# Kernel tuning notes

Hardware: AMD Instinct MI355X
Metric: run time of the kernel (lower is better)

Reference implementation:

```python
import jax, jax.numpy as jnp
import numpy as np

HEADS = 12
D_MODEL = 768
D_K = D_MODEL // HEADS


def setup_inputs() -> dict:
    key = jax.random.key(0)
    ks = jax.random.split(key, 11)
    B, S, D = 2, 2048, D_MODEL
    s = 1.0 / np.sqrt(D)
    return {
        "query": jax.random.normal(ks[0], (B, S, D), jnp.float32),
        "key": jax.random.normal(ks[1], (B, S, D), jnp.float32),
        "value": jax.random.normal(ks[2], (B, S, D), jnp.float32),
        "Wq": jax.random.normal(ks[3], (D, D), jnp.float32) * s,
        "bq": jnp.zeros((D,), jnp.float32),
        "Wk": jax.random.normal(ks[4], (D, D), jnp.float32) * s,
        "bk": jnp.zeros((D,), jnp.float32),
        "Wv": jax.random.normal(ks[5], (D, D), jnp.float32) * s,
        "bv": jnp.zeros((D,), jnp.float32),
        "Wo": jax.random.normal(ks[6], (D, D), jnp.float32) * s,
        "bo": jnp.zeros((D,), jnp.float32),
    }


def reference(query, key, value, Wq, bq, Wk, bk, Wv, bv, Wo, bo):
    B, S, D = query.shape
    # linear projections (weights stored as [in, out])
    q = query @ Wq + bq
    k = key @ Wk + bk
    v = value @ Wv + bv
    # [B, H, S, d_k]
    q = q.reshape(B, S, HEADS, D_K).transpose(0, 2, 1, 3)
    k = k.reshape(B, S, HEADS, D_K).transpose(0, 2, 1, 3)
    v = v.reshape(B, S, HEADS, D_K).transpose(0, 2, 1, 3)
    # scores: note module scales by sqrt(d_k) (key.size(-1)), not self.scaled
    scores = jnp.einsum("bhqd,bhkd->bhqk", q, k) / jnp.sqrt(jnp.asarray(D_K, q.dtype))
    weights = jax.nn.softmax(scores, axis=-1)
    context = jnp.einsum("bhqk,bhkd->bhqd", weights, v)
    context = context.transpose(0, 2, 1, 3).reshape(B, S, D)
    return context @ Wo + bo
```

## Files before the change

### kernel.cpp

```cpp
#include <hip/hip_runtime.h>
#include <hip/hip_bf16.h>
#include <math.h>

#define D_MODEL 768
#define HEADS 12
#define DK 64
#define SEQ 2048
#define BATCH 2
#define MTOT (BATCH * SEQ)
#define QSCALE 0.18033688011112042f

using short8 = __attribute__((ext_vector_type(8))) short;
using us4    = __attribute__((ext_vector_type(4))) unsigned short;
using f32x4  = __attribute__((ext_vector_type(4))) float;
using f32x16 = __attribute__((ext_vector_type(16))) float;

static __device__ __forceinline__ unsigned f2bf2(float x, float y) {
    __hip_bfloat162 t = __float22bfloat162_rn(float2{x, y});
    return *reinterpret_cast<unsigned*>(&t);
}
static __device__ __forceinline__ unsigned short f2bf1(float x) {
    __hip_bfloat16 t = __float2bfloat16(x);
    return *reinterpret_cast<unsigned short*>(&t);
}
static __device__ __forceinline__ float bf2f(unsigned short u) {
    unsigned v = (unsigned)u << 16;
    return __uint_as_float(v);
}
static __device__ __forceinline__ short8 cvt8(float4 a, float4 b) {
    union { unsigned u[4]; short8 s; } r;
    r.u[0] = f2bf2(a.x, a.y);
    r.u[1] = f2bf2(a.z, a.w);
    r.u[2] = f2bf2(b.x, b.y);
    r.u[3] = f2bf2(b.z, b.w);
    return r.s;
}
static __device__ __forceinline__ float fast_exp2(float x) {
#if __has_builtin(__builtin_amdgcn_exp2f)
    return __builtin_amdgcn_exp2f(x);
#else
    return __expf(x * 0.6931471805599453f);
#endif
}
static __device__ __forceinline__ unsigned pk2(float lo, float hi) {
    unsigned d;
    asm("v_cvt_pk_bf16_f32 %0, %1, %2" : "=v"(d) : "v"(lo), "v"(hi));
    return d;
}

static __device__ __forceinline__ void gload_lds16(const void* g, void* l) {
    __builtin_amdgcn_global_load_lds(
        (const __attribute__((address_space(1))) void*)g,
        (__attribute__((address_space(3))) void*)l, 16, 0, 0);
}

static __device__ __forceinline__ void barrier_lgkm() {
    asm volatile("s_waitcnt lgkmcnt(0)" ::: "memory");
    __builtin_amdgcn_s_barrier();
    __builtin_amdgcn_sched_barrier(0);
}
static __device__ __forceinline__ void barrier_vm0() {
    asm volatile("s_waitcnt vmcnt(0)" ::: "memory");
    __builtin_amdgcn_s_barrier();
    __builtin_amdgcn_sched_barrier(0);
}

__global__ __launch_bounds__(256) void cvt_wt_k(
    const float* __restrict__ Wq, const float* __restrict__ Wk,
    const float* __restrict__ Wv, const float* __restrict__ Wo,
    unsigned short* __restrict__ Wqt, unsigned short* __restrict__ Wkt,
    unsigned short* __restrict__ Wvt, unsigned short* __restrict__ Wot)
{
    const int z = blockIdx.z;
    const float* W = z == 0 ? Wq : z == 1 ? Wk : z == 2 ? Wv : Wo;
    unsigned short* Wt = z == 0 ? Wqt : z == 1 ? Wkt : z == 2 ? Wvt : Wot;
    __shared__ float t[32][33];
    const int n0 = blockIdx.x * 32, k0 = blockIdx.y * 32;
    const int tx = threadIdx.x & 31;
    const int ty0 = (threadIdx.x >> 5) * 4;
    #pragma unroll
    for (int j = 0; j < 4; ++j)
        t[ty0 + j][tx] = W[(size_t)(k0 + ty0 + j) * D_MODEL + n0 + tx];
    __syncthreads();
    #pragma unroll
    for (int j = 0; j < 4; ++j)
        Wt[(size_t)(n0 + ty0 + j) * D_MODEL + k0 + tx] = f2bf1(t[tx][ty0 + j]);
}

__global__ __launch_bounds__(512) void gemm_qkv_k(
    const float* __restrict__ query, const float* __restrict__ key,
    const float* __restrict__ value,
    const unsigned short* __restrict__ Wqt, const unsigned short* __restrict__ Wkt,
    const unsigned short* __restrict__ Wvt,
    const float* __restrict__ bq, const float* __restrict__ bk,
    const float* __restrict__ bv,
    unsigned short* __restrict__ qb, unsigned short* __restrict__ kb,
    unsigned short* __restrict__ vb)
{
    __shared__ __align__(16) char gsm[65536];

    const int bid = blockIdx.x;
    const int xcd = bid & 7;
    const int idx = bid >> 3;
    const int z   = idx / 24;
    const int rr  = idx % 24;
    const int brow = (xcd * 4 + rr / 6) * 128;
    const int bcol = (rr % 6) * 128;

    const float* A           = z == 0 ? query : z == 1 ? key : value;
    const unsigned short* Wt = z == 0 ? Wqt : z == 1 ? Wkt : Wvt;
    const float* bias        = z == 0 ? bq  : z == 1 ? bk  : bv;
    unsigned short* C        = z == 0 ? qb  : z == 1 ? kb  : vb;
    const float scale        = z == 0 ? QSCALE : 1.0f;

    const int tid  = threadIdx.x;
    const int w    = tid >> 6;
    const int lane = tid & 63;
    const int g    = lane >> 4, c = lane & 15;
    const int wr   = w >> 2, wc = w & 3;

    f32x4 acc[4][2] = {};

    const int xc  = (c & 7) << 4;
    const int rb0 = c * 128 + ((g * 16) ^ xc);
    const int rb1 = c * 128 + ((64 + g * 16) ^ xc);

    int bsrow[2], bsoff[2], bsdst[2];
    #pragma unroll
    for (int r = 0; r < 2; ++r) {
        int phys = (w * 2 + r) * 1024 + lane * 16;
        int row  = phys >> 7;
        int slot = (phys >> 4) & 7;
        bsrow[r] = row;
        bsoff[r] = (slot ^ (row & 7)) * 8;
        bsdst[r] = (w * 2 + r) * 1024;
    }
    const int ar = tid >> 2;
    const int ac = (tid & 3) << 4;
    int awa[2];
    #pragma unroll
    for (int i = 0; i < 2; ++i)
        awa[i] = ar * 128 + (((ac << 1) + 16 * i) ^ ((ar & 7) << 4));
    const float* Ap32 = A + (size_t)(brow + ar) * D_MODEL + ac;

    float4 ra0, ra1, ra2, ra3;

    auto stageB = [&](int k0, int buf) {
        #pragma unroll
        for (int r = 0; r < 2; ++r)
            gload_lds16(Wt + (size_t)(bcol + bsrow[r]) * D_MODEL + k0 + bsoff[r],
                        gsm + 32768 + buf * 16384 + bsdst[r]);
    };
    auto loadA32 = [&](int k0) {
        ra0 = *(const float4*)(Ap32 + k0);
        ra1 = *(const float4*)(Ap32 + k0 + 4);
        ra2 = *(const float4*)(Ap32 + k0 + 8);
        ra3 = *(const float4*)(Ap32 + k0 + 12);
    };
    auto writeA32 = [&](int buf) {
        *(short8*)(gsm + buf * 16384 + awa[0]) = cvt8(ra0, ra1);
        *(short8*)(gsm + buf * 16384 + awa[1]) = cvt8(ra2, ra3);
    };

    stageB(0, 0);
    loadA32(0);
    writeA32(0);
    barrier_lgkm();

    for (int k0 = 0; k0 < D_MODEL; k0 += 128) {
        #pragma unroll
        for (int u = 0; u < 2; ++u) {
            const int kn = min(k0 + u * 64 + 64, D_MODEL - 64);
            stageB(kn, u ^ 1);
            loadA32(kn);
            __builtin_amdgcn_sched_barrier(0);

            __builtin_amdgcn_s_setprio(1);
            #pragma unroll
            for (int kstep = 0; kstep < 2; ++kstep) {
                const int rb = kstep ? rb1 : rb0;
                short8 af[4], bf[2];
                #pragma unroll
                for (int m = 0; m < 4; ++m)
                    af[m] = *(const short8*)(gsm + u * 16384 + wr * 8192 +
                                             m * 2048 + rb);
                #pragma unroll
                for (int n = 0; n < 2; ++n)
                    bf[n] = *(const short8*)(gsm + 32768 + u * 16384 +
                                             wc * 4096 + n * 2048 + rb);
                #pragma unroll
                for (int m = 0; m < 4; ++m)
                    #pragma unroll
                    for (int n = 0; n < 2; ++n)
                        acc[m][n] = __builtin_amdgcn_mfma_f32_16x16x32_bf16(
                                        af[m], bf[n], acc[m][n], 0, 0, 0);
            }
            __builtin_amdgcn_s_setprio(0);

            writeA32(u ^ 1);
            barrier_lgkm();
        }
    }

    #pragma unroll
    for (int m = 0; m < 4; ++m)
        #pragma unroll
        for (int n = 0; n < 2; ++n) {
            const int col = bcol + wc * 32 + n * 16 + c;
            const float bval = bias[col];
            #pragma unroll
            for (int j = 0; j < 4; ++j) {
                const int row = brow + wr * 64 + m * 16 + g * 4 + j;
                C[(size_t)row * D_MODEL + col] = f2bf1((acc[m][n][j] + bval) * scale);
            }
        }
}

__global__ __launch_bounds__(256) void gemm_o_k(
    const unsigned short* __restrict__ A, const unsigned short* __restrict__ Wt,
    const float* __restrict__ bias, float* __restrict__ C)
{
    __shared__ __align__(16) char gsm[32768];

    const int bid = blockIdx.x;
    const int xcd = bid & 7;
    const int idx = bid >> 3;
    const int brow = (xcd * 8 + idx / 12) * 64;
    const int bcol = (idx % 12) * 64;

    const int tid  = threadIdx.x;
    const int w    = tid >> 6;
    const int lane = tid & 63;
    const int g    = lane >> 4, c = lane & 15;
    const int wr   = w >> 1, wc = w & 1;

    f32x4 acc[2][2] = {{f32x4{0,0,0,0}, f32x4{0,0,0,0}},
                       {f32x4{0,0,0,0}, f32x4{0,0,0,0}}};

    const int xc  = (c & 7) << 4;
    const int rb0 = c * 128 + ((g * 16) ^ xc);
    const int rb1 = c * 128 + ((64 + g * 16) ^ xc);
    const int a0 = rb0 + wr * 4096, a1 = rb1 + wr * 4096;
    const int b0r = rb0 + 16384 + wc * 4096, b1r = rb1 + 16384 + wc * 4096;

    int bsrow[2], bsoff[2], bsdst[2];
    #pragma unroll
    for (int r = 0; r < 2; ++r) {
        int phys = (w + 4 * r) * 1024 + lane * 16;
        int row  = phys >> 7;
        int slot = (phys >> 4) & 7;
        bsrow[r] = row;
        bsoff[r] = (slot ^ (row & 7)) * 8;
        bsdst[r] = (w + 4 * r) * 1024;
    }

    auto stage = [&](int k0, int buf) {
        #pragma unroll
        for (int r = 0; r < 2; ++r) {
            gload_lds16(A  + (size_t)(brow + bsrow[r]) * D_MODEL + k0 + bsoff[r],
                        gsm + buf * 8192 + bsdst[r]);
            gload_lds16(Wt + (size_t)(bcol + bsrow[r]) * D_MODEL + k0 + bsoff[r],
                        gsm + 16384 + buf * 8192 + bsdst[r]);
        }
    };

    stage(0, 0);
    barrier_vm0();

    for (int k0 = 0; k0 < D_MODEL; k0 += 128) {
        #pragma unroll
        for (int u = 0; u < 2; ++u) {
            const int kn = min(k0 + u * 64 + 64, D_MODEL - 64);
            stage(kn, u ^ 1);
            __builtin_amdgcn_sched_barrier(0);

            #pragma unroll
            for (int kstep = 0; kstep < 2; ++kstep) {
                short8 af[2], bf[2];
                #pragma unroll
                for (int m = 0; m < 2; ++m)
                    af[m] = *(const short8*)(gsm + u * 8192 + m * 2048 +
                                             (kstep ? a1 : a0));
                #pragma unroll
                for (int n = 0; n < 2; ++n)
                    bf[n] = *(const short8*)(gsm + u * 8192 + n * 2048 +
                                             (kstep ? b1r : b0r));
                #pragma unroll
                for (int m = 0; m < 2; ++m)
                    #pragma unroll
                    for (int n = 0; n < 2; ++n)
                        acc[m][n] = __builtin_amdgcn_mfma_f32_16x16x32_bf16(
                                        af[m], bf[n], acc[m][n], 0, 0, 0);
            }
            barrier_vm0();
        }
    }

    #pragma unroll
    for (int m = 0; m < 2; ++m)
        #pragma unroll
        for (int n = 0; n < 2; ++n) {
            const int col = bcol + wc * 32 + n * 16 + c;
            const float bval = bias[col];
            #pragma unroll
            for (int j = 0; j < 4; ++j) {
                const int row = brow + wr * 32 + m * 16 + g * 4 + j;
                C[(size_t)row * D_MODEL + col] = acc[m][n][j] + bval;
            }
        }
}

__global__ __launch_bounds__(256) void attn_mfma_k(
    const unsigned short* __restrict__ q, const unsigned short* __restrict__ k,
    const unsigned short* __restrict__ v, unsigned short* __restrict__ opart,
    float* __restrict__ mpart, float* __restrict__ lpart)
{
    __shared__ __align__(16) char sm[32768];

    const int tid  = threadIdx.x;
    const int w    = tid >> 6;
    const int lane = tid & 63;
    const int c    = lane & 31;
    const int hi   = lane >> 5;

    const int bid  = blockIdx.x;
    const int swz  = (bid & 7) * 96 + (bid >> 3);
    const int qt   = swz & 15;
    const int rest = swz >> 4;
    const int half = rest & 1;
    const int hb   = rest >> 1;
    const int h    = hb % HEADS;
    const int b    = hb / HEADS;
    const int q0   = qt * 128;
    const int NT2  = 16;

    short8 qf[4];
    {
        const unsigned short* qp =
            q + (size_t)(b * SEQ + q0 + w * 32 + c) * D_MODEL + h * DK;
        #pragma unroll
        for (int t = 0; t < 4; ++t)
            qf[t] = *(const short8*)(qp + t * 16 + hi * 8);
    }

    float m_run = -INFINITY;
    f32x16 lacc = {};
    f32x16 o0 = {}, o1 = {};
    const short8 ONES = {0x3F80, 0x3F80, 0x3F80, 0x3F80,
                         0x3F80, 0x3F80, 0x3F80, 0x3F80};

    const int xc = (c & 7) << 4;
    int koff[4];
    #pragma unroll
    for (int t = 0; t < 4; ++t)
        koff[t] = ((32 * t + 16 * hi) ^ xc) + c * 128;

    int kdst[2];
    const unsigned short* kg[2];
    {
        const unsigned short* kbase =
            k + (size_t)(b * SEQ + half * (SEQ / 2)) * D_MODEL + h * DK;
        #pragma unroll
        for (int r = 0; r < 2; ++r) {
            int phys = (w + 4 * r) * 1024 + lane * 16;
            int row  = phys >> 7;
            int slot = (phys >> 4) & 7;
            kdst[r]  = (w + 4 * r) * 1024;
            kg[r]    = kbase + (size_t)row * D_MODEL + (slot ^ (row & 7)) * 8;
        }
    }
    const int cv = tid & 15, vd0 = (tid >> 4) << 2;
    const int vposP = 16 * (cv >> 3) + 8 * ((cv >> 2) & 1) + 2 * (cv & 3);
    int vwa[4];
    #pragma unroll
    for (int j = 0; j < 4; ++j) {
        const int row = vd0 + j;
        vwa[j] = 16384 + row * 128 + ((2 * vposP) ^ ((row & 7) << 4));
    }
    const unsigned short* vg =
        v + (size_t)(b * SEQ + half * (SEQ / 2) + cv) * D_MODEL + h * DK + vd0;
    const int TS = 64 * D_MODEL;

    us4 va, vb_, vc, vd;

    auto issue_k = [&](int buf) {
        gload_lds16(kg[0], sm + buf * 8192 + kdst[0]);
        gload_lds16(kg[1], sm + buf * 8192 + kdst[1]);
        kg[0] += TS; kg[1] += TS;
    };
    auto load_v = [&]() {
        va  = *(const us4*)(vg);
        vb_ = *(const us4*)(vg + 16 * D_MODEL);
        vc  = *(const us4*)(vg + 32 * D_MODEL);
        vd  = *(const us4*)(vg + 48 * D_MODEL);
        vg += TS;
    };
    auto write_v = [&](int buf) {
        #pragma unroll
        for (int j = 0; j < 4; ++j) {
            unsigned lo  = (unsigned)va[j]  | ((unsigned)vc[j] << 16);
            unsigned hi2 = (unsigned)vb_[j] | ((unsigned)vd[j] << 16);
            *(unsigned*)(sm + buf * 8192 + vwa[j])        = lo;
            *(unsigned*)(sm + buf * 8192 + (vwa[j] ^ 64)) = hi2;
        }
    };

    issue_k(0);
    __builtin_amdgcn_sched_barrier(0);
    load_v();
    write_v(0);
    barrier_lgkm();

    for (int kt2 = 0; kt2 < NT2; kt2 += 2) {
        #pragma unroll
        for (int u = 0; u < 2; ++u) {
            const int tile = kt2 + u;
            issue_k(u ^ 1);
            __builtin_amdgcn_sched_barrier(0);
            load_v();
            __builtin_amdgcn_sched_barrier(0);

            f32x16 s0 = {}, s1 = {};
            __builtin_amdgcn_s_setprio(1);
            #pragma unroll
            for (int t = 0; t < 4; ++t) {
                short8 kf0 = *(const short8*)(sm + u * 8192 + koff[t]);
                short8 kf1 = *(const short8*)(sm + u * 8192 + 4096 + koff[t]);
                s0 = __builtin_amdgcn_mfma_f32_32x32x16_bf16(kf0, qf[t], s0, 0, 0, 0);
                s1 = __builtin_amdgcn_mfma_f32_32x32x16_bf16(kf1, qf[t], s1, 0, 0, 0);
            }
            __builtin_amdgcn_s_setprio(0);

            float rmax = s0[0];
            #pragma unroll
            for (int r = 1; r < 16; ++r) rmax = fmaxf(rmax, s0[r]);
            #pragma unroll
            for (int r = 0; r < 16; ++r) rmax = fmaxf(rmax, s1[r]);
            rmax = fmaxf(rmax, __shfl_xor(rmax, 32));

            if (tile == 0) {
                m_run = rmax;
            } else if (__any(rmax > m_run + 11.0f)) {
                const float mnew = fmaxf(m_run, rmax);
                const float sc = fast_exp2(m_run - mnew);
                m_run = mnew;
                #pragma unroll
                for (int r = 0; r < 16; ++r) {
                    const float scr = __shfl(sc, (r & 3) + 8 * (r >> 2) + 4 * hi);
                    lacc[r] *= scr;
                    o0[r] *= scr;
                    o1[r] *= scr;
                }
            }

            #pragma unroll
            for (int r = 0; r < 16; ++r) {
                s0[r] = fast_exp2(s0[r] - m_run);
                s1[r] = fast_exp2(s1[r] - m_run);
            }

            __builtin_amdgcn_s_setprio(1);
            #pragma unroll
            for (int t = 0; t < 4; ++t) {
                union { unsigned u4[4]; short8 s8; } pf;
                #pragma unroll
                for (int j = 0; j < 4; ++j)
                    pf.u4[j] = pk2(s0[4 * t + j], s1[4 * t + j]);
                short8 vf0 = *(const short8*)(sm + 16384 + u * 8192 + koff[t]);
                short8 vf1 = *(const short8*)(sm + 16384 + u * 8192 + 4096 + koff[t]);
                lacc = __builtin_amdgcn_mfma_f32_32x32x16_bf16(pf.s8, ONES, lacc, 0, 0, 0);
                o0 = __builtin_amdgcn_mfma_f32_32x32x16_bf16(pf.s8, vf0, o0, 0, 0, 0);
                o1 = __builtin_amdgcn_mfma_f32_32x32x16_bf16(pf.s8, vf1, o1, 0, 0, 0);
            }
            __builtin_amdgcn_s_setprio(0);

            write_v(u ^ 1);
            barrier_lgkm();
        }
    }

    const size_t obase = (size_t)half * ((size_t)MTOT * D_MODEL) +
                         (size_t)(b * SEQ) * D_MODEL + h * DK;
    #pragma unroll
    for (int r = 0; r < 16; ++r) {
        const int qrow = q0 + w * 32 + (r & 3) + 8 * (r >> 2) + 4 * hi;
        unsigned short* ob = opart + obase + (size_t)qrow * D_MODEL;
        ob[c]      = f2bf1(o0[r]);
        ob[32 + c] = f2bf1(o1[r]);
    }
    const size_t mlbase = (size_t)half * MTOT * HEADS +
                          (size_t)(b * SEQ) * HEADS + h;
    if (hi == 0)
        mpart[mlbase + (size_t)(q0 + w * 32 + c) * HEADS] = m_run;
    if (c == 0) {
        #pragma unroll
        for (int r = 0; r < 16; ++r) {
            const int qrow = q0 + w * 32 + (r & 3) + 8 * (r >> 2) + 4 * hi;
            lpart[mlbase + (size_t)qrow * HEADS] = lacc[r];
        }
    }
}

__global__ __launch_bounds__(256) void combine_k(
    const unsigned short* __restrict__ op, const float* __restrict__ mp,
    const float* __restrict__ lp, unsigned short* __restrict__ cb)
{
    const int t   = blockIdx.x * 256 + threadIdx.x;
    const int row = t / 96;
    const int gi  = t - row * 96;
    const int col = gi << 3;
    const int h   = gi >> 3;

    const float m0 = mp[(size_t)row * HEADS + h];
    const float m1 = mp[(size_t)MTOT * HEADS + (size_t)row * HEADS + h];
    const float l0 = lp[(size_t)row * HEADS + h];
    const float l1 = lp[(size_t)MTOT * HEADS + (size_t)row * HEADS + h];
    const float m  = fmaxf(m0, m1);
    const float s0 = fast_exp2(m0 - m);
    const float s1 = fast_exp2(m1 - m);
    const float inv = 1.0f / (l0 * s0 + l1 * s1);
    const float a0 = s0 * inv, a1 = s1 * inv;

    const size_t off = (size_t)row * D_MODEL + col;
    us4 x0  = *(const us4*)(op + off);
    us4 x0b = *(const us4*)(op + off + 4);
    us4 x1  = *(const us4*)(op + (size_t)MTOT * D_MODEL + off);
    us4 x1b = *(const us4*)(op + (size_t)MTOT * D_MODEL + off + 4);

    union { unsigned short u[8]; short8 s; } r;
    #pragma unroll
    for (int j = 0; j < 4; ++j) {
        r.u[j]     = f2bf1(bf2f(x0[j])  * a0 + bf2f(x1[j])  * a1);
        r.u[4 + j] = f2bf1(bf2f(x0b[j]) * a0 + bf2f(x1b[j]) * a1);
    }
    *(short8*)(cb + off) = r.s;
}

extern "C" void kernel_launch(void* const* d_in, const int* in_sizes, int n_in,
                              void* d_out, int out_size, void* d_ws, size_t ws_size,
                              hipStream_t stream) {
    const float* query = (const float*)d_in[0];
    const float* key   = (const float*)d_in[1];
    const float* value = (const float*)d_in[2];
    const float* Wq = (const float*)d_in[3];
    const float* bq = (const float*)d_in[4];
    const float* Wk = (const float*)d_in[5];
    const float* bk = (const float*)d_in[6];
    const float* Wv = (const float*)d_in[7];
    const float* bv = (const float*)d_in[8];
    const float* Wo = (const float*)d_in[9];
    const float* bo = (const float*)d_in[10];
    float* out = (float*)d_out;

    const size_t mat = (size_t)MTOT * D_MODEL;
    unsigned short* qb  = (unsigned short*)d_ws;
    unsigned short* kb  = qb + mat;
    unsigned short* vb  = kb + mat;
    unsigned short* cb  = vb + mat;
    unsigned short* Wqt = cb + mat;
    unsigned short* Wkt = Wqt + (size_t)D_MODEL * D_MODEL;
    unsigned short* Wvt = Wkt + (size_t)D_MODEL * D_MODEL;
    unsigned short* Wot = Wvt + (size_t)D_MODEL * D_MODEL;
    unsigned short* op  = Wot + (size_t)D_MODEL * D_MODEL;
    float*          mp  = (float*)(op + 2 * mat);
    float*          lp  = mp + 2 * (size_t)MTOT * HEADS;

    cvt_wt_k<<<dim3(D_MODEL / 32, D_MODEL / 32, 4), 256, 0, stream>>>(
        Wq, Wk, Wv, Wo, Wqt, Wkt, Wvt, Wot);

    gemm_qkv_k<<<dim3(576), 512, 0, stream>>>(
        query, key, value, Wqt, Wkt, Wvt, bq, bk, bv, qb, kb, vb);

    attn_mfma_k<<<dim3(768), 256, 0, stream>>>(qb, kb, vb, op, mp, lp);

    combine_k<<<dim3(MTOT * D_MODEL / 8 / 256), 256, 0, stream>>>(op, mp, lp, cb);

    gemm_o_k<<<dim3(768), 256, 0, stream>>>(cb, Wot, bo, out);
}
```

Measured before the change: 104.8 us.

## Split attention KV range four ways and widen combine to four partials

Result: slower. 108.3 us (+3.3%).

```diff
diff --git a/kernel.cpp b/kernel.cpp
--- a/kernel.cpp
+++ b/kernel.cpp
@@ -46,6 +46,9 @@
     unsigned d;
     asm("v_cvt_pk_bf16_f32 %0, %1, %2" : "=v"(d) : "v"(lo), "v"(hi));
     return d;
+}
+static __device__ __forceinline__ int sg(int x) {
+    return (((x & 3) << 1) | ((x >> 2) & 1)) ^ ((x >> 3) & 3);
 }
 
 static __device__ __forceinline__ void gload_lds16(const void* g, void* l) {
@@ -324,15 +327,14 @@
     const int hi   = lane >> 5;
 
     const int bid  = blockIdx.x;
-    const int swz  = (bid & 7) * 96 + (bid >> 3);
+    const int swz  = (bid & 7) * 192 + (bid >> 3);
     const int qt   = swz & 15;
-    const int rest = swz >> 4;
-    const int half = rest & 1;
-    const int hb   = rest >> 1;
+    const int half = (swz >> 4) & 3;
+    const int hb   = swz >> 6;
     const int h    = hb % HEADS;
     const int b    = hb / HEADS;
     const int q0   = qt * 128;
-    const int NT2  = 16;
+    const int NT2  = 8;
 
     short8 qf[4];
     {
@@ -349,24 +351,23 @@
     const short8 ONES = {0x3F80, 0x3F80, 0x3F80, 0x3F80,
                          0x3F80, 0x3F80, 0x3F80, 0x3F80};
 
-    const int xc = (c & 7) << 4;
     int koff[4];
     #pragma unroll
     for (int t = 0; t < 4; ++t)
-        koff[t] = ((32 * t + 16 * hi) ^ xc) + c * 128;
+        koff[t] = ((32 * t + 16 * hi) ^ (sg(c) << 4)) + c * 128;
 
     int kdst[2];
     const unsigned short* kg[2];
     {
         const unsigned short* kbase =
-            k + (size_t)(b * SEQ + half * (SEQ / 2)) * D_MODEL + h * DK;
+            k + (size_t)(b * SEQ + half * (SEQ / 4)) * D_MODEL + h * DK;
         #pragma unroll
         for (int r = 0; r < 2; ++r) {
             int phys = (w + 4 * r) * 1024 + lane * 16;
             int row  = phys >> 7;
             int slot = (phys >> 4) & 7;
             kdst[r]  = (w + 4 * r) * 1024;
-            kg[r]    = kbase + (size_t)row * D_MODEL + (slot ^ (row & 7)) * 8;
+            kg[r]    = kbase + (size_t)row * D_MODEL + (slot ^ sg(row)) * 8;
         }
     }
     const int cv = tid & 15, vd0 = (tid >> 4) << 2;
@@ -375,10 +376,10 @@
     #pragma unroll
     for (int j = 0; j < 4; ++j) {
         const int row = vd0 + j;
-        vwa[j] = 16384 + row * 128 + ((2 * vposP) ^ ((row & 7) << 4));
+        vwa[j] = 16384 + row * 128 + ((2 * vposP) ^ (sg(row) << 4));
     }
     const unsigned short* vg =
-        v + (size_t)(b * SEQ + half * (SEQ / 2) + cv) * D_MODEL + h * DK + vd0;
+        v + (size_t)(b * SEQ + half * (SEQ / 4) + cv) * D_MODEL + h * DK + vd0;
     const int TS = 64 * D_MODEL;
 
     us4 va, vb_, vc, vd;
@@ -511,28 +512,38 @@
     const int col = gi << 3;
     const int h   = gi >> 3;
 
-    const float m0 = mp[(size_t)row * HEADS + h];
-    const float m1 = mp[(size_t)MTOT * HEADS + (size_t)row * HEADS + h];
-    const float l0 = lp[(size_t)row * HEADS + h];
-    const float l1 = lp[(size_t)MTOT * HEADS + (size_t)row * HEADS + h];
-    const float m  = fmaxf(m0, m1);
-    const float s0 = fast_exp2(m0 - m);
-    const float s1 = fast_exp2(m1 - m);
-    const float inv = 1.0f / (l0 * s0 + l1 * s1);
-    const float a0 = s0 * inv, a1 = s1 * inv;
+    float mv[4], lv[4];
+    #pragma unroll
+    for (int i = 0; i < 4; ++i) {
+        mv[i] = mp[(size_t)i * MTOT * HEADS + (size_t)row * HEADS + h];
+        lv[i] = lp[(size_t)i * MTOT * HEADS + (size_t)row * HEADS + h];
+    }
+    const float m = fmaxf(fmaxf(mv[0], mv[1]), fmaxf(mv[2], mv[3]));
+    float a[4], lsum = 0.f;
+    #pragma unroll
+    for (int i = 0; i < 4; ++i) {
+        a[i] = fast_exp2(mv[i] - m);
+        lsum += lv[i] * a[i];
+    }
+    const float inv = 1.0f / lsum;
+    #pragma unroll
+    for (int i = 0; i < 4; ++i) a[i] *= inv;
 
     const size_t off = (size_t)row * D_MODEL + col;
-    us4 x0  = *(const us4*)(op + off);
-    us4 x0b = *(const us4*)(op + off + 4);
-    us4 x1  = *(const us4*)(op + (size_t)MTOT * D_MODEL + off);
-    us4 x1b = *(const us4*)(op + (size_t)MTOT * D_MODEL + off + 4);
-
+    float acc[8] = {};
+    #pragma unroll
+    for (int i = 0; i < 4; ++i) {
+        us4 x0 = *(const us4*)(op + (size_t)i * MTOT * D_MODEL + off);
+        us4 x1 = *(const us4*)(op + (size_t)i * MTOT * D_MODEL + off + 4);
+        #pragma unroll
+        for (int j = 0; j < 4; ++j) {
+            acc[j]     += bf2f(x0[j]) * a[i];
+            acc[4 + j] += bf2f(x1[j]) * a[i];
+        }
+    }
     union { unsigned short u[8]; short8 s; } r;
     #pragma unroll
-    for (int j = 0; j < 4; ++j) {
-        r.u[j]     = f2bf1(bf2f(x0[j])  * a0 + bf2f(x1[j])  * a1);
-        r.u[4 + j] = f2bf1(bf2f(x0b[j]) * a0 + bf2f(x1b[j]) * a1);
-    }
+    for (int j = 0; j < 8; ++j) r.u[j] = f2bf1(acc[j]);
     *(short8*)(cb + off) = r.s;
 }
 
@@ -553,17 +564,18 @@
     float* out = (float*)d_out;
 
     const size_t mat = (size_t)MTOT * D_MODEL;
+    const size_t D2  = (size_t)D_MODEL * D_MODEL;
     unsigned short* qb  = (unsigned short*)d_ws;
     unsigned short* kb  = qb + mat;
     unsigned short* vb  = kb + mat;
-    unsigned short* cb  = vb + mat;
-    unsigned short* Wqt = cb + mat;
-    unsigned short* Wkt = Wqt + (size_t)D_MODEL * D_MODEL;
-    unsigned short* Wvt = Wkt + (size_t)D_MODEL * D_MODEL;
-    unsigned short* Wot = Wvt + (size_t)D_MODEL * D_MODEL;
-    unsigned short* op  = Wot + (size_t)D_MODEL * D_MODEL;
-    float*          mp  = (float*)(op + 2 * mat);
-    float*          lp  = mp + 2 * (size_t)MTOT * HEADS;
+    unsigned short* Wqt = vb + mat;
+    unsigned short* Wkt = Wqt + D2;
+    unsigned short* Wvt = Wkt + D2;
+    unsigned short* Wot = Wvt + D2;
+    unsigned short* op  = Wot + D2;
+    float*          mp  = (float*)Wqt;
+    float*          lp  = mp + 4 * (size_t)MTOT * HEADS;
+    unsigned short* cb  = qb;
 
     cvt_wt_k<<<dim3(D_MODEL / 32, D_MODEL / 32, 4), 256, 0, stream>>>(
         Wq, Wk, Wv, Wo, Wqt, Wkt, Wvt, Wot);
@@ -571,7 +583,7 @@
     gemm_qkv_k<<<dim3(576), 512, 0, stream>>>(
         query, key, value, Wqt, Wkt, Wvt, bq, bk, bv, qb, kb, vb);
 
-    attn_mfma_k<<<dim3(768), 256, 0, stream>>>(qb, kb, vb, op, mp, lp);
+    attn_mfma_k<<<dim3(1536), 256, 0, stream>>>(qb, kb, vb, op, mp, lp);
 
     combine_k<<<dim3(MTOT * D_MODEL / 8 / 256), 256, 0, stream>>>(op, mp, lp, cb);
 
```

## Software-pipeline attention: overlap QK of next tile with softmax-PV of previous

Applied to the files above, without the earlier changes.

After: 107.0 us. 2.0% more time.

```diff
diff --git a/kernel.cpp b/kernel.cpp
--- a/kernel.cpp
+++ b/kernel.cpp
@@ -315,7 +315,7 @@
     const unsigned short* __restrict__ v, unsigned short* __restrict__ opart,
     float* __restrict__ mpart, float* __restrict__ lpart)
 {
-    __shared__ __align__(16) char sm[32768];
+    __shared__ __align__(16) char sm[49152];
 
     const int tid  = threadIdx.x;
     const int w    = tid >> 6;
@@ -332,7 +332,6 @@
     const int h    = hb % HEADS;
     const int b    = hb / HEADS;
     const int q0   = qt * 128;
-    const int NT2  = 16;
 
     short8 qf[4];
     {
@@ -375,7 +374,7 @@
     #pragma unroll
     for (int j = 0; j < 4; ++j) {
         const int row = vd0 + j;
-        vwa[j] = 16384 + row * 128 + ((2 * vposP) ^ ((row & 7) << 4));
+        vwa[j] = row * 128 + ((2 * vposP) ^ ((row & 7) << 4));
     }
     const unsigned short* vg =
         v + (size_t)(b * SEQ + half * (SEQ / 2) + cv) * D_MODEL + h * DK + vd0;
@@ -395,14 +394,65 @@
         vd  = *(const us4*)(vg + 48 * D_MODEL);
         vg += TS;
     };
-    auto write_v = [&](int buf) {
+    auto write_v = [&](int vbuf) {
         #pragma unroll
         for (int j = 0; j < 4; ++j) {
             unsigned lo  = (unsigned)va[j]  | ((unsigned)vc[j] << 16);
             unsigned hi2 = (unsigned)vb_[j] | ((unsigned)vd[j] << 16);
-            *(unsigned*)(sm + buf * 8192 + vwa[j])        = lo;
-            *(unsigned*)(sm + buf * 8192 + (vwa[j] ^ 64)) = hi2;
-        }
+            *(unsigned*)(sm + 16384 + vbuf * 8192 + vwa[j])        = lo;
+            *(unsigned*)(sm + 16384 + vbuf * 8192 + (vwa[j] ^ 64)) = hi2;
+        }
+    };
+    auto qk = [&](int kbuf, f32x16& d0, f32x16& d1) {
+        __builtin_amdgcn_s_setprio(1);
+        #pragma unroll
+        for (int t = 0; t < 4; ++t) {
+            short8 kf0 = *(const short8*)(sm + kbuf * 8192 + koff[t]);
+            short8 kf1 = *(const short8*)(sm + kbuf * 8192 + 4096 + koff[t]);
+            d0 = __builtin_amdgcn_mfma_f32_32x32x16_bf16(kf0, qf[t], d0, 0, 0, 0);
+            d1 = __builtin_amdgcn_mfma_f32_32x32x16_bf16(kf1, qf[t], d1, 0, 0, 0);
+        }
+        __builtin_amdgcn_s_setprio(0);
+    };
+    auto softmax_pv = [&](f32x16& sp0, f32x16& sp1, int vbuf) {
+        float rmax = sp0[0];
+        #pragma unroll
+        for (int r = 1; r < 16; ++r) rmax = fmaxf(rmax, sp0[r]);
+        #pragma unroll
+        for (int r = 0; r < 16; ++r) rmax = fmaxf(rmax, sp1[r]);
+        rmax = fmaxf(rmax, __shfl_xor(rmax, 32));
+
+        if (__any(rmax > m_run + 11.0f)) {
+            const float mnew = fmaxf(m_run, rmax);
+            const float sc = fast_exp2(m_run - mnew);
+            m_run = mnew;
+            #pragma unroll
+            for (int r = 0; r < 16; ++r) {
+                const float scr = __shfl(sc, (r & 3) + 8 * (r >> 2) + 4 * hi);
+                lacc[r] *= scr;
+                o0[r] *= scr;
+                o1[r] *= scr;
+            }
+        }
+        #pragma unroll
+        for (int r = 0; r < 16; ++r) {
+            sp0[r] = fast_exp2(sp0[r] - m_run);
+            sp1[r] = fast_exp2(sp1[r] - m_run);
+        }
+        __builtin_amdgcn_s_setprio(1);
+        #pragma unroll
+        for (int t = 0; t < 4; ++t) {
+            union { unsigned u4[4]; short8 s8; } pf;
+            #pragma unroll
+            for (int j = 0; j < 4; ++j)
+                pf.u4[j] = pk2(sp0[4 * t + j], sp1[4 * t + j]);
+            short8 vf0 = *(const short8*)(sm + 16384 + vbuf * 8192 + koff[t]);
+            short8 vf1 = *(const short8*)(sm + 16384 + vbuf * 8192 + 4096 + koff[t]);
+            lacc = __builtin_amdgcn_mfma_f32_32x32x16_bf16(pf.s8, ONES, lacc, 0, 0, 0);
+            o0 = __builtin_amdgcn_mfma_f32_32x32x16_bf16(pf.s8, vf0, o0, 0, 0, 0);
+            o1 = __builtin_amdgcn_mfma_f32_32x32x16_bf16(pf.s8, vf1, o1, 0, 0, 0);
+        }
+        __builtin_amdgcn_s_setprio(0);
     };
 
     issue_k(0);
@@ -411,73 +461,28 @@
     write_v(0);
     barrier_lgkm();
 
-    for (int kt2 = 0; kt2 < NT2; kt2 += 2) {
-        #pragma unroll
-        for (int u = 0; u < 2; ++u) {
-            const int tile = kt2 + u;
-            issue_k(u ^ 1);
+    f32x16 sE0 = {}, sE1 = {}, sO0 = {}, sO1 = {};
+    for (int kt2 = 0; kt2 < 16; kt2 += 4) {
+        #pragma unroll
+        for (int u = 0; u < 4; ++u) {
+            issue_k((u + 1) & 1);
             __builtin_amdgcn_sched_barrier(0);
             load_v();
             __builtin_amdgcn_sched_barrier(0);
 
-            f32x16 s0 = {}, s1 = {};
-            __builtin_amdgcn_s_setprio(1);
-            #pragma unroll
-            for (int t = 0; t < 4; ++t) {
-                short8 kf0 = *(const short8*)(sm + u * 8192 + koff[t]);
-                short8 kf1 = *(const short8*)(sm + u * 8192 + 4096 + koff[t]);
-                s0 = __builtin_amdgcn_mfma_f32_32x32x16_bf16(kf0, qf[t], s0, 0, 0, 0);
-                s1 = __builtin_amdgcn_mfma_f32_32x32x16_bf16(kf1, qf[t], s1, 0, 0, 0);
+            if (u & 1) { sO0 = f32x16{}; sO1 = f32x16{}; qk(u & 1, sO0, sO1); }
+            else       { sE0 = f32x16{}; sE1 = f32x16{}; qk(u & 1, sE0, sE1); }
+
+            if (kt2 + u > 0) {
+                if (u & 1) softmax_pv(sE0, sE1, (u + 3) & 3);
+                else       softmax_pv(sO0, sO1, (u + 3) & 3);
             }
-            __builtin_amdgcn_s_setprio(0);
-
-            float rmax = s0[0];
-            #pragma unroll
-            for (int r = 1; r < 16; ++r) rmax = fmaxf(rmax, s0[r]);
-            #pragma unroll
-            for (int r = 0; r < 16; ++r) rmax = fmaxf(rmax, s1[r]);
-            rmax = fmaxf(rmax, __shfl_xor(rmax, 32));
-
-            if (tile == 0) {
-                m_run = rmax;
-            } else if (__any(rmax > m_run + 11.0f)) {
-                const float mnew = fmaxf(m_run, rmax);
-                const float sc = fast_exp2(m_run - mnew);
-                m_run = mnew;
-                #pragma unroll
-                for (int r = 0; r < 16; ++r) {
-                    const float scr = __shfl(sc, (r & 3) + 8 * (r >> 2) + 4 * hi);
-                    lacc[r] *= scr;
-                    o0[r] *= scr;
-                    o1[r] *= scr;
-                }
-            }
-
-            #pragma unroll
-            for (int r = 0; r < 16; ++r) {
-                s0[r] = fast_exp2(s0[r] - m_run);
-                s1[r] = fast_exp2(s1[r] - m_run);
-            }
-
-            __builtin_amdgcn_s_setprio(1);
-            #pragma unroll
-            for (int t = 0; t < 4; ++t) {
-                union { unsigned u4[4]; short8 s8; } pf;
-                #pragma unroll
-                for (int j = 0; j < 4; ++j)
-                    pf.u4[j] = pk2(s0[4 * t + j], s1[4 * t + j]);
-                short8 vf0 = *(const short8*)(sm + 16384 + u * 8192 + koff[t]);
-                short8 vf1 = *(const short8*)(sm + 16384 + u * 8192 + 4096 + koff[t]);
-                lacc = __builtin_amdgcn_mfma_f32_32x32x16_bf16(pf.s8, ONES, lacc, 0, 0, 0);
-                o0 = __builtin_amdgcn_mfma_f32_32x32x16_bf16(pf.s8, vf0, o0, 0, 0, 0);
-                o1 = __builtin_amdgcn_mfma_f32_32x32x16_bf16(pf.s8, vf1, o1, 0, 0, 0);
-            }
-            __builtin_amdgcn_s_setprio(0);
-
-            write_v(u ^ 1);
+
+            write_v((u + 1) & 3);
             barrier_lgkm();
         }
     }
+    softmax_pv(sO0, sO1, 3);
 
     const size_t obase = (size_t)half * ((size_t)MTOT * D_MODEL) +
                          (size_t)(b * SEQ) * D_MODEL + h * DK;
```

## Fuse split-KV combine into output projection GEMM A-tile load

Applied to the files above, without the earlier changes.

Result: slower. 110.1 us (+5.0%).

```diff
diff --git a/kernel.cpp b/kernel.cpp
--- a/kernel.cpp
+++ b/kernel.cpp
@@ -12,6 +12,7 @@
 
 using short8 = __attribute__((ext_vector_type(8))) short;
 using us4    = __attribute__((ext_vector_type(4))) unsigned short;
+using us8    = __attribute__((ext_vector_type(8))) unsigned short;
 using f32x4  = __attribute__((ext_vector_type(4))) float;
 using f32x16 = __attribute__((ext_vector_type(16))) float;
 
@@ -217,7 +218,8 @@
 }
 
 __global__ __launch_bounds__(256) void gemm_o_k(
-    const unsigned short* __restrict__ A, const unsigned short* __restrict__ Wt,
+    const unsigned short* __restrict__ op, const float* __restrict__ mp,
+    const float* __restrict__ lp, const unsigned short* __restrict__ Wt,
     const float* __restrict__ bias, float* __restrict__ C)
 {
     __shared__ __align__(16) char gsm[32768];
@@ -240,7 +242,7 @@
     const int xc  = (c & 7) << 4;
     const int rb0 = c * 128 + ((g * 16) ^ xc);
     const int rb1 = c * 128 + ((64 + g * 16) ^ xc);
-    const int a0 = rb0 + wr * 4096, a1 = rb1 + wr * 4096;
+    const int a0r = rb0 + wr * 4096, a1r = rb1 + wr * 4096;
     const int b0r = rb0 + 16384 + wc * 4096, b1r = rb1 + 16384 + wc * 4096;
 
     int bsrow[2], bsoff[2], bsdst[2];
@@ -253,34 +255,76 @@
         bsoff[r] = (slot ^ (row & 7)) * 8;
         bsdst[r] = (w + 4 * r) * 1024;
     }
-
-    auto stage = [&](int k0, int buf) {
-        #pragma unroll
-        for (int r = 0; r < 2; ++r) {
-            gload_lds16(A  + (size_t)(brow + bsrow[r]) * D_MODEL + k0 + bsoff[r],
-                        gsm + buf * 8192 + bsdst[r]);
+    const int ar = tid >> 2;
+    const int ac = (tid & 3) << 4;
+    int awa[2];
+    #pragma unroll
+    for (int i = 0; i < 2; ++i)
+        awa[i] = ar * 128 + (((ac << 1) + 16 * i) ^ ((ar & 7) << 4));
+    const int arow = brow + ar;
+    const unsigned short* op0 = op + (size_t)arow * D_MODEL + ac;
+    const unsigned short* op1 = op0 + (size_t)MTOT * D_MODEL;
+
+    us8 x0, x0h, x1, x1h;
+    float a0f, a1f;
+
+    auto stageB = [&](int k0, int buf) {
+        #pragma unroll
+        for (int r = 0; r < 2; ++r)
             gload_lds16(Wt + (size_t)(bcol + bsrow[r]) * D_MODEL + k0 + bsoff[r],
                         gsm + 16384 + buf * 8192 + bsdst[r]);
-        }
-    };
-
-    stage(0, 0);
-    barrier_vm0();
+    };
+    auto loadA = [&](int k0) {
+        x0  = *(const us8*)(op0 + k0);
+        x0h = *(const us8*)(op0 + k0 + 8);
+        x1  = *(const us8*)(op1 + k0);
+        x1h = *(const us8*)(op1 + k0 + 8);
+        const int hh = k0 >> 6;
+        const float m0 = mp[(size_t)arow * HEADS + hh];
+        const float m1 = mp[(size_t)MTOT * HEADS + (size_t)arow * HEADS + hh];
+        const float l0 = lp[(size_t)arow * HEADS + hh];
+        const float l1 = lp[(size_t)MTOT * HEADS + (size_t)arow * HEADS + hh];
+        const float m  = fmaxf(m0, m1);
+        const float s0 = fast_exp2(m0 - m);
+        const float s1 = fast_exp2(m1 - m);
+        const float inv = 1.0f / (l0 * s0 + l1 * s1);
+        a0f = s0 * inv;
+        a1f = s1 * inv;
+    };
+    auto writeA = [&](int buf) {
+        union { unsigned u[4]; short8 s; } rA, rB;
+        #pragma unroll
+        for (int j = 0; j < 4; ++j) {
+            rA.u[j] = f2bf2(bf2f(x0[2*j])   * a0f + bf2f(x1[2*j])   * a1f,
+                            bf2f(x0[2*j+1]) * a0f + bf2f(x1[2*j+1]) * a1f);
+            rB.u[j] = f2bf2(bf2f(x0h[2*j])   * a0f + bf2f(x1h[2*j])   * a1f,
+                            bf2f(x0h[2*j+1]) * a0f + bf2f(x1h[2*j+1]) * a1f);
+        }
+        *(short8*)(gsm + buf * 8192 + awa[0]) = rA.s;
+        *(short8*)(gsm + buf * 8192 + awa[1]) = rB.s;
+    };
+
+    stageB(0, 0);
+    loadA(0);
+    writeA(0);
+    barrier_lgkm();
 
     for (int k0 = 0; k0 < D_MODEL; k0 += 128) {
         #pragma unroll
         for (int u = 0; u < 2; ++u) {
             const int kn = min(k0 + u * 64 + 64, D_MODEL - 64);
-            stage(kn, u ^ 1);
+            stageB(kn, u ^ 1);
+            loadA(kn);
             __builtin_amdgcn_sched_barrier(0);
 
+            __builtin_amdgcn_s_setprio(1);
             #pragma unroll
             for (int kstep = 0; kstep < 2; ++kstep) {
                 short8 af[2], bf[2];
                 #pragma unroll
                 for (int m = 0; m < 2; ++m)
                     af[m] = *(const short8*)(gsm + u * 8192 + m * 2048 +
-                                             (kstep ? a1 : a0));
+                                             (kstep ? a1r : a0r));
                 #pragma unroll
                 for (int n = 0; n < 2; ++n)
                     bf[n] = *(const short8*)(gsm + u * 8192 + n * 2048 +
@@ -292,7 +336,10 @@
                         acc[m][n] = __builtin_amdgcn_mfma_f32_16x16x32_bf16(
                                         af[m], bf[n], acc[m][n], 0, 0, 0);
             }
-            barrier_vm0();
+            __builtin_amdgcn_s_setprio(0);
+
+            writeA(u ^ 1);
+            barrier_lgkm();
         }
     }
 
@@ -499,41 +546,6 @@
             lpart[mlbase + (size_t)qrow * HEADS] = lacc[r];
         }
     }
-}
-
-__global__ __launch_bounds__(256) void combine_k(
-    const unsigned short* __restrict__ op, const float* __restrict__ mp,
-    const float* __restrict__ lp, unsigned short* __restrict__ cb)
-{
-    const int t   = blockIdx.x * 256 + threadIdx.x;
-    const int row = t / 96;
-    const int gi  = t - row * 96;
-    const int col = gi << 3;
-    const int h   = gi >> 3;
-
-    const float m0 = mp[(size_t)row * HEADS + h];
-    const float m1 = mp[(size_t)MTOT * HEADS + (size_t)row * HEADS + h];
-    const float l0 = lp[(size_t)row * HEADS + h];
-    const float l1 = lp[(size_t)MTOT * HEADS + (size_t)row * HEADS + h];
-    const float m  = fmaxf(m0, m1);
-    const float s0 = fast_exp2(m0 - m);
-    const float s1 = fast_exp2(m1 - m);
-    const float inv = 1.0f / (l0 * s0 + l1 * s1);
-    const float a0 = s0 * inv, a1 = s1 * inv;
-
-    const size_t off = (size_t)row * D_MODEL + col;
-    us4 x0  = *(const us4*)(op + off);
-    us4 x0b = *(const us4*)(op + off + 4);
-    us4 x1  = *(const us4*)(op + (size_t)MTOT * D_MODEL + off);
-    us4 x1b = *(const us4*)(op + (size_t)MTOT * D_MODEL + off + 4);
-
-    union { unsigned short u[8]; short8 s; } r;
-    #pragma unroll
-    for (int j = 0; j < 4; ++j) {
-        r.u[j]     = f2bf1(bf2f(x0[j])  * a0 + bf2f(x1[j])  * a1);
-        r.u[4 + j] = f2bf1(bf2f(x0b[j]) * a0 + bf2f(x1b[j]) * a1);
-    }
-    *(short8*)(cb + off) = r.s;
 }
 
 extern "C" void kernel_launch(void* const* d_in, const int* in_sizes, int n_in,
@@ -564,6 +576,7 @@
     unsigned short* op  = Wot + (size_t)D_MODEL * D_MODEL;
     float*          mp  = (float*)(op + 2 * mat);
     float*          lp  = mp + 2 * (size_t)MTOT * HEADS;
+    (void)cb;
 
     cvt_wt_k<<<dim3(D_MODEL / 32, D_MODEL / 32, 4), 256, 0, stream>>>(
         Wq, Wk, Wv, Wo, Wqt, Wkt, Wvt, Wot);
@@ -573,7 +586,5 @@
 
     attn_mfma_k<<<dim3(768), 256, 0, stream>>>(qb, kb, vb, op, mp, lp);
 
-    combine_k<<<dim3(MTOT * D_MODEL / 8 / 256), 256, 0, stream>>>(op, mp, lp, cb);
-
-    gemm_o_k<<<dim3(768), 256, 0, stream>>>(cb, Wot, bo, out);
-}
+    gemm_o_k<<<dim3(768), 256, 0, stream>>>(op, mp, lp, Wot, bo, out);
+}
```
